# Performance work log

Hardware: AMD Instinct MI355X
Metric: run time of the kernel (lower is better)

The kernel has to match this reference:

```python
import jax, jax.numpy as jnp
import numpy as np

EPS = 1e-5
TAU = 2.0
NUM_HEADS = 8
SCALE = 0.125

# Heaviside spike with sigmoid surrogate gradient (spikingjelly default, alpha=4)
@jax.custom_vjp
def spike_fn(x):
    return (x >= 0).astype(x.dtype)

def _spike_fwd(x):
    return spike_fn(x), x

def _spike_bwd(x, g):
    alpha = 4.0
    s = jax.nn.sigmoid(alpha * x)
    return (g * alpha * s * (1.0 - s),)

spike_fn.defvjp(_spike_fwd, _spike_bwd)

def lif(x, v_th):
    # MultiStepLIFNode: v += (x - v)/tau; spike = H(v - v_th); hard reset v=0 (detach_reset)
    def step(v, xt):
        v = v + (xt - v) / TAU
        s = spike_fn(v - v_th)
        v = v * (1.0 - jax.lax.stop_gradient(s))
        return v, s
    _, s = jax.lax.scan(step, jnp.zeros_like(x[0]), x)
    return s

def bn(y, g, b, m, rv):
    # BatchNorm1d in eval mode over channel dim C (last dim here, since torch code
    # transposes to (TB,C,N) before BN and back after)
    return (y - m) * (g * jax.lax.rsqrt(rv + EPS)) + b

def setup_inputs():
    key = jax.random.key(0)
    T, B, N, C = 4, 8, 512, 512
    ks = jax.random.split(key, 16)
    d = {"x": jax.random.normal(ks[0], (T, B, N, C), jnp.float32)}
    i = 1
    for name in ("q", "k", "v", "p"):
        d[f"w{name}"] = jax.random.normal(ks[i], (C, C), jnp.float32) * 0.02; i += 1
        d[f"b{name}"] = jnp.zeros((C,), jnp.float32)
        d[f"g{name}"] = jnp.ones((C,), jnp.float32)
        d[f"beta{name}"] = jnp.zeros((C,), jnp.float32)
        d[f"m{name}"] = jax.random.normal(ks[i], (C,), jnp.float32) * 0.1; i += 1
        d[f"rv{name}"] = jax.random.uniform(ks[i], (C,), jnp.float32, minval=0.5, maxval=1.5); i += 1
    return d

def reference(x, wq, bq, gq, betaq, mq, rvq,
              wk, bk, gk, betak, mk, rvk,
              wv, bv, gv, betav, mv, rvv,
              wp, bp, gp, betap, mp, rvp):
    T, B, N, C = x.shape
    H = NUM_HEADS
    D = C // H
    xf = x.reshape(T * B, N, C)

    def branch(w, b, g, be, m, rv):
        # Linear -> BN(eval) -> LIF -> split heads
        # (k/v paths in the torch code reshape to (T,B,C,N) between BN and LIF, but
        # since those are pure reshapes of the same flat buffer and LIF is elementwise
        # per timestep, the math is identical to the q path.)
        y = bn(jnp.einsum('bnc,oc->bno', xf, w) + b, g, be, m, rv).reshape(T, B, N, C)
        s = lif(y, 1.0)
        return s.reshape(T, B, N, H, D).transpose(0, 1, 3, 2, 4)  # (T,B,H,N,D)

    q = branch(wq, bq, gq, betaq, mq, rvq)
    k = branch(wk, bk, gk, betak, mk, rvk)
    v = branch(wv, bv, gv, betav, mv, rvv)

    attn = jnp.einsum('tbhnd,tbhmd->tbhnm', q, k) * SCALE  # no softmax
    o = jnp.einsum('tbhnm,tbhmd->tbhnd', attn, v)
    o = o.transpose(0, 1, 3, 2, 4).reshape(T, B, N, C)
    o = lif(o, 0.5)  # attn_lif, v_threshold=0.5

    y = bn(jnp.einsum('bnc,oc->bno', o.reshape(T * B, N, C), wp) + bp,
           gp, betap, mp, rvp).reshape(T, B, N, C)
    return lif(y, 1.0)  # proj_lif
```

## Files before the change

### kernel.cpp

```cpp
#include <hip/hip_runtime.h>
#include <hip/hip_bf16.h>

typedef _Float16 h8 __attribute__((ext_vector_type(8)));
typedef float f4 __attribute__((ext_vector_type(4)));

#define T_ 4
#define B_ 8
#define N_ 512
#define C_ 512
#define H_ 8
#define D_ 64
#define BNR 4096
#define EPSf 1e-5f
#define F16_MIN_NORM 6.1035156e-05f
#define INV4096 0.000244140625f

__global__ __launch_bounds__(256)
void split_pack_x(const float* __restrict__ in, _Float16* __restrict__ h1,
                  _Float16* __restrict__ h2)
{
    const int gid = blockIdx.x * 256 + threadIdx.x;
    const int lane = gid & 63;
    const int ks = (gid >> 6) & 15;
    const int t = (gid >> 10) & 3;
    const int rt = gid >> 12;
    const int row = rt * 16 + (lane & 15);
    const size_t src = ((size_t)t * BNR + row) * C_ + ks * 32 + (lane >> 4) * 8;
    const float4 x0 = *reinterpret_cast<const float4*>(in + src);
    const float4 x1 = *reinterpret_cast<const float4*>(in + src + 4);
    h8 a, b;
    #pragma unroll
    for (int j = 0; j < 8; ++j) {
        const float xv = (j < 4) ? (&x0.x)[j] : (&x1.x)[j - 4];
        const float hi = (fabsf(xv) >= F16_MIN_NORM) ? xv : 0.0f;
        const _Float16 h = (_Float16)hi;
        const float r = (xv - (float)h) * 4096.0f;
        a[j] = h; b[j] = (_Float16)r;
    }
    *reinterpret_cast<h8*>(h1 + (size_t)gid * 8) = a;
    *reinterpret_cast<h8*>(h2 + (size_t)gid * 8) = b;
}

__device__ __forceinline__
void pack_w_one(const float* __restrict__ W, _Float16* __restrict__ Wp1,
                _Float16* __restrict__ Wp2, int gid)
{
    const int lane = gid & 63;
    const int ni = (gid >> 6) & 3;
    const int ks = (gid >> 8) & 15;
    const int ct = gid >> 12;
    const int col = ct * 64 + ni * 16 + (lane & 15);
    const int k = ks * 32 + (lane >> 4) * 8;
    const float* src = W + (size_t)col * C_ + k;
    h8 a, b;
    #pragma unroll
    for (int j = 0; j < 8; ++j) {
        const float xv = src[j];
        const float hi = (fabsf(xv) >= F16_MIN_NORM) ? xv : 0.0f;
        const _Float16 h = (_Float16)hi;
        const float r = (xv - (float)h) * 4096.0f;
        a[j] = h; b[j] = (_Float16)r;
    }
    *reinterpret_cast<h8*>(Wp1 + (size_t)gid * 8) = a;
    *reinterpret_cast<h8*>(Wp2 + (size_t)gid * 8) = b;
}

__global__ __launch_bounds__(256)
void pack_w_all(const float* __restrict__ Wq, const float* __restrict__ Wk,
                const float* __restrict__ Wv, const float* __restrict__ Wp,
                _Float16* q1, _Float16* q2, _Float16* k1, _Float16* k2,
                _Float16* v1, _Float16* v2, _Float16* p1, _Float16* p2)
{
    const int g = blockIdx.x * 256 + threadIdx.x;
    const int br = g >> 15;
    const int gid = g & 32767;
    if (br == 0)      pack_w_one(Wq, q1, q2, gid);
    else if (br == 1) pack_w_one(Wk, k1, k2, gid);
    else if (br == 2) pack_w_one(Wv, v1, v2, gid);
    else              pack_w_one(Wp, p1, p2, gid);
}

__global__ __launch_bounds__(512, 4)
void gemm3_bn_lif(const _Float16* __restrict__ A1p, const _Float16* __restrict__ A2p,
                  const _Float16* __restrict__ Wq1, const _Float16* __restrict__ Wq2,
                  const _Float16* __restrict__ Wk1, const _Float16* __restrict__ Wk2,
                  const _Float16* __restrict__ Wv1, const _Float16* __restrict__ Wv2,
                  const float* __restrict__ biq, const float* __restrict__ gaq,
                  const float* __restrict__ beq, const float* __restrict__ meq,
                  const float* __restrict__ rvq,
                  const float* __restrict__ bik, const float* __restrict__ gak,
                  const float* __restrict__ bek, const float* __restrict__ mek,
                  const float* __restrict__ rvk,
                  const float* __restrict__ biv, const float* __restrict__ gav,
                  const float* __restrict__ bev, const float* __restrict__ mev,
                  const float* __restrict__ rvv,
                  _Float16* __restrict__ oq, _Float16* __restrict__ ok,
                  _Float16* __restrict__ ov)
{
    __shared__ __align__(16) char wsm[16384];
    const int br = blockIdx.y;
    const _Float16* W1 = (br == 0) ? Wq1 : (br == 1) ? Wk1 : Wv1;
    const _Float16* W2 = (br == 0) ? Wq2 : (br == 1) ? Wk2 : Wv2;
    const float* bias = (br == 0) ? biq : (br == 1) ? bik : biv;
    const float* gam  = (br == 0) ? gaq : (br == 1) ? gak : gav;
    const float* bet  = (br == 0) ? beq : (br == 1) ? bek : bev;
    const float* mea  = (br == 0) ? meq : (br == 1) ? mek : mev;
    const float* rva  = (br == 0) ? rvq : (br == 1) ? rvk : rvv;
    _Float16* out = (br == 0) ? oq : (br == 1) ? ok : ov;

    const int id = blockIdx.x;
    const int bt = (id & 7) * 8 + ((id >> 3) & 7);
    const int ct = id >> 6;
    const int tid = threadIdx.x;
    const int wave = tid >> 6, lane = tid & 63;
    const int tp = wave & 1, wr = wave >> 1;
    const int rt = bt * 4 + wr;
    const int row0 = bt * 64, col0 = ct * 64;
    const int lr = lane & 15, lk = lane >> 4;

    f4 accA[2][4], accB[2][4];
    #pragma unroll
    for (int ti = 0; ti < 2; ++ti)
        #pragma unroll
        for (int ni = 0; ni < 4; ++ni) { accA[ti][ni] = (f4)0.0f; accB[ti][ni] = (f4)0.0f; }

    const _Float16* aB1 = A1p + (size_t)rt * 32768 + lane * 8;
    const _Float16* aB2 = A2p + (size_t)rt * 32768 + lane * 8;
    const int s_ = wave >> 2, q_ = wave & 3;
    const _Float16* wsrc = (s_ ? W2 : W1) + (size_t)ct * 32768 + q_ * 512 + lane * 8;
    const int wdoff = s_ * 4096 + q_ * 1024;

    auto stageW = [&](int ks, int b) {
        __builtin_amdgcn_global_load_lds(
            (const __attribute__((address_space(1))) unsigned int*)(wsrc + ks * 2048),
            (__attribute__((address_space(3))) unsigned int*)(wsm + b * 8192 + wdoff),
            16, 0, 0);
    };

    stageW(0, 0);
    h8 a1c[2], a2c[2];
    #pragma unroll
    for (int ti = 0; ti < 2; ++ti) {
        const int t = tp * 2 + ti;
        a1c[ti] = *reinterpret_cast<const h8*>(aB1 + (t * 16 + 0) * 512);
        a2c[ti] = *reinterpret_cast<const h8*>(aB2 + (t * 16 + 0) * 512);
    }
    #pragma unroll
    for (int ks = 0; ks < 16; ++ks) {
        const int buf = ks & 1;
        asm volatile("s_waitcnt vmcnt(4)" ::: "memory");
        __builtin_amdgcn_s_barrier();
        __builtin_amdgcn_sched_barrier(0);
        h8 a1n[2], a2n[2];
        if (ks < 15) {
            stageW(ks + 1, buf ^ 1);
            #pragma unroll
            for (int ti = 0; ti < 2; ++ti) {
                const int t = tp * 2 + ti;
                a1n[ti] = *reinterpret_cast<const h8*>(aB1 + (t * 16 + ks + 1) * 512);
                a2n[ti] = *reinterpret_cast<const h8*>(aB2 + (t * 16 + ks + 1) * 512);
            }
        }
        const char* wb = wsm + buf * 8192;
        #pragma unroll
        for (int ni = 0; ni < 4; ++ni) {
            const h8 wf1 = *reinterpret_cast<const h8*>(wb + ni * 1024 + lane * 16);
            const h8 wf2 = *reinterpret_cast<const h8*>(wb + 4096 + ni * 1024 + lane * 16);
            #pragma unroll
            for (int ti = 0; ti < 2; ++ti) {
                accA[ti][ni] = __builtin_amdgcn_mfma_f32_16x16x32_f16(a1c[ti], wf1, accA[ti][ni], 0, 0, 0);
                accB[ti][ni] = __builtin_amdgcn_mfma_f32_16x16x32_f16(a1c[ti], wf2, accB[ti][ni], 0, 0, 0);
                accB[ti][ni] = __builtin_amdgcn_mfma_f32_16x16x32_f16(a2c[ti], wf1, accB[ti][ni], 0, 0, 0);
            }
        }
        if (ks < 15) {
            #pragma unroll
            for (int ti = 0; ti < 2; ++ti) { a1c[ti] = a1n[ti]; a2c[ti] = a2n[ti]; }
        }
    }

    float* vst = (float*)wsm;
    float sc[4], bi[4], mn[4], be[4];
    #pragma unroll
    for (int ni = 0; ni < 4; ++ni) {
        const int c = col0 + ni * 16 + lr;
        sc[ni] = gam[c] * (1.0f / sqrtf(rva[c] + EPSf));
        bi[ni] = bias[c]; mn[ni] = mea[c]; be[ni] = bet[c];
    }
    __syncthreads();
    if (tp == 0) {
        #pragma unroll
        for (int ni = 0; ni < 4; ++ni)
            #pragma unroll
            for (int r = 0; r < 4; ++r) {
                const int rl = wr * 16 + lk * 4 + r;
                const int bn = row0 + rl;
                float vm = 0.0f;
                #pragma unroll
                for (int ti = 0; ti < 2; ++ti) {
                    const float res = accA[ti][ni][r] + INV4096 * accB[ti][ni][r];
                    const float y = ((res + bi[ni]) - mn[ni]) * sc[ni] + be[ni];
                    vm = vm + (y - vm) * 0.5f;
                    const float s = (vm >= 1.0f) ? 1.0f : 0.0f;
                    vm = (s != 0.0f) ? 0.0f : vm;
                    const int b = bn >> 9, n = bn & 511;
                    out[((((size_t)ti * B_ + b) * H_ + ct) * N_ + n) * D_ + ni * 16 + lr] =
                        (_Float16)s;
                }
                vst[rl * 64 + ni * 16 + lr] = vm;
            }
    }
    __syncthreads();
    if (tp == 1) {
        #pragma unroll
        for (int ni = 0; ni < 4; ++ni)
            #pragma unroll
            for (int r = 0; r < 4; ++r) {
                const int rl = wr * 16 + lk * 4 + r;
                const int bn = row0 + rl;
                float vm = vst[rl * 64 + ni * 16 + lr];
                #pragma unroll
                for (int ti = 0; ti < 2; ++ti) {
                    const float res = accA[ti][ni][r] + INV4096 * accB[ti][ni][r];
                    const float y = ((res + bi[ni]) - mn[ni]) * sc[ni] + be[ni];
                    vm = vm + (y - vm) * 0.5f;
                    const float s = (vm >= 1.0f) ? 1.0f : 0.0f;
                    vm = (s != 0.0f) ? 0.0f : vm;
                    const int b = bn >> 9, n = bn & 511;
                    out[((((size_t)(2 + ti) * B_ + b) * H_ + ct) * N_ + n) * D_ + ni * 16 + lr] =
                        (_Float16)s;
                }
            }
    }
}

__global__ __launch_bounds__(512, 4)
void gemm_p_bn_lif(const _Float16* __restrict__ A1p,
                   const _Float16* __restrict__ Wp1, const _Float16* __restrict__ Wp2,
                   const float* __restrict__ bias, const float* __restrict__ gam,
                   const float* __restrict__ bet, const float* __restrict__ mea,
                   const float* __restrict__ rva, float* __restrict__ out_plain)
{
    __shared__ __align__(16) char wsm[65536];
    const int id = blockIdx.x;
    const int bt = (id & 7) * 8 + ((id >> 3) & 7);
    const int ct = id >> 6;
    const int tid = threadIdx.x;
    const int wave = tid >> 6, lane = tid & 63;
    const int tp = wave & 1, wr = wave >> 1;
    const int rt = bt * 4 + wr;
    const int row0 = bt * 64, col0 = ct * 64;
    const int lr = lane & 15, lk = lane >> 4;

    f4 accA[2][4], accB[2][4];
    #pragma unroll
    for (int ti = 0; ti < 2; ++ti)
        #pragma unroll
        for (int ni = 0; ni < 4; ++ni) { accA[ti][ni] = (f4)0.0f; accB[ti][ni] = (f4)0.0f; }

    const _Float16* aB1 = A1p + (size_t)rt * 32768 + lane * 8;
    const int s_ = wave >> 2, q_ = wave & 3;
    const _Float16* wsrc = (s_ ? Wp2 : Wp1) + (size_t)ct * 32768 + q_ * 512 + lane * 8;
    const int wdoff = s_ * 4096 + q_ * 1024;

    auto stageChunk = [&](int c, int b) {
        #pragma unroll
        for (int ksl = 0; ksl < 4; ++ksl) {
            __builtin_amdgcn_global_load_lds(
                (const __attribute__((address_space(1))) unsigned int*)(wsrc + (c * 4 + ksl) * 2048),
                (__attribute__((address_space(3))) unsigned int*)(wsm + b * 32768 + ksl * 8192 + wdoff),
                16, 0, 0);
        }
    };

    stageChunk(0, 0);
    #pragma unroll
    for (int c = 0; c < 4; ++c) {
        const int buf = c & 1;
        __syncthreads();
        if (c < 3) stageChunk(c + 1, buf ^ 1);
        #pragma unroll
        for (int ksl = 0; ksl < 4; ++ksl) {
            const int ks = c * 4 + ksl;
            h8 a1[2];
            #pragma unroll
            for (int ti = 0; ti < 2; ++ti) {
                const int t = tp * 2 + ti;
                a1[ti] = *reinterpret_cast<const h8*>(aB1 + (t * 16 + ks) * 512);
            }
            const char* wb = wsm + buf * 32768 + ksl * 8192;
            #pragma unroll
            for (int ni = 0; ni < 4; ++ni) {
                const h8 wf1 = *reinterpret_cast<const h8*>(wb + ni * 1024 + lane * 16);
                const h8 wf2 = *reinterpret_cast<const h8*>(wb + 4096 + ni * 1024 + lane * 16);
                #pragma unroll
                for (int ti = 0; ti < 2; ++ti) {
                    accA[ti][ni] = __builtin_amdgcn_mfma_f32_16x16x32_f16(a1[ti], wf1, accA[ti][ni], 0, 0, 0);
                    accB[ti][ni] = __builtin_amdgcn_mfma_f32_16x16x32_f16(a1[ti], wf2, accB[ti][ni], 0, 0, 0);
                }
            }
        }
    }

    float* vst = (float*)wsm;
    float sc[4], bi[4], mn[4], be[4];
    #pragma unroll
    for (int ni = 0; ni < 4; ++ni) {
        const int c = col0 + ni * 16 + lr;
        sc[ni] = gam[c] * (1.0f / sqrtf(rva[c] + EPSf));
        bi[ni] = bias[c]; mn[ni] = mea[c]; be[ni] = bet[c];
    }
    __syncthreads();
    if (tp == 0) {
        #pragma unroll
        for (int ni = 0; ni < 4; ++ni)
            #pragma unroll
            for (int r = 0; r < 4; ++r) {
                const int rl = wr * 16 + lk * 4 + r;
                const int bn = row0 + rl;
                float vm = 0.0f;
                #pragma unroll
                for (int ti = 0; ti < 2; ++ti) {
                    const float res = accA[ti][ni][r] + INV4096 * accB[ti][ni][r];
                    const float y = ((res + bi[ni]) - mn[ni]) * sc[ni] + be[ni];
                    vm = vm + (y - vm) * 0.5f;
                    const float s = (vm >= 1.0f) ? 1.0f : 0.0f;
                    vm = (s != 0.0f) ? 0.0f : vm;
                    out_plain[((size_t)ti * BNR + bn) * C_ + col0 + ni * 16 + lr] = s;
                }
                vst[rl * 64 + ni * 16 + lr] = vm;
            }
    }
    __syncthreads();
    if (tp == 1) {
        #pragma unroll
        for (int ni = 0; ni < 4; ++ni)
            #pragma unroll
            for (int r = 0; r < 4; ++r) {
                const int rl = wr * 16 + lk * 4 + r;
                const int bn = row0 + rl;
                float vm = vst[rl * 64 + ni * 16 + lr];
                #pragma unroll
                for (int ti = 0; ti < 2; ++ti) {
                    const float res = accA[ti][ni][r] + INV4096 * accB[ti][ni][r];
                    const float y = ((res + bi[ni]) - mn[ni]) * sc[ni] + be[ni];
                    vm = vm + (y - vm) * 0.5f;
                    const float s = (vm >= 1.0f) ? 1.0f : 0.0f;
                    vm = (s != 0.0f) ? 0.0f : vm;
                    out_plain[((size_t)(2 + ti) * BNR + bn) * C_ + col0 + ni * 16 + lr] = s;
                }
            }
    }
}

__global__ __launch_bounds__(256)
void ktv_kernel(const _Float16* __restrict__ sk, const _Float16* __restrict__ sv,
                _Float16* __restrict__ kvT)
{
    __shared__ _Float16 kl[64][64];
    __shared__ _Float16 vl[64][64];
    const int tbh = blockIdx.x;
    const int tid = threadIdx.x;
    const int tx = tid & 15, ty = tid >> 4;
    const size_t base = (size_t)tbh * N_ * D_;
    float acc[4][4] = {};
    for (int n0 = 0; n0 < N_; n0 += 64) {
        __syncthreads();
        #pragma unroll
        for (int p = 0; p < 2; ++p) {
            const int idx = tid + p * 256;
            const int r = idx >> 3, c8 = (idx & 7) * 8;
            *reinterpret_cast<float4*>(&kl[r][c8]) =
                *reinterpret_cast<const float4*>(&sk[base + (size_t)(n0 + r) * D_ + c8]);
            *reinterpret_cast<float4*>(&vl[r][c8]) =
                *reinterpret_cast<const float4*>(&sv[base + (size_t)(n0 + r) * D_ + c8]);
        }
        __syncthreads();
        for (int nn = 0; nn < 64; ++nn) {
            float a[4], b[4];
            #pragma unroll
            for (int i = 0; i < 4; ++i) a[i] = (float)kl[nn][ty * 4 + i];
            #pragma unroll
            for (int j = 0; j < 4; ++j) b[j] = (float)vl[nn][tx * 4 + j];
            #pragma unroll
            for (int i = 0; i < 4; ++i)
                #pragma unroll
                for (int j = 0; j < 4; ++j)
                    acc[i][j] = fmaf(a[i], b[j], acc[i][j]);
        }
    }
    _Float16* out = kvT + (size_t)tbh * 4096;
    #pragma unroll
    for (int i = 0; i < 4; ++i)
        #pragma unroll
        for (int j = 0; j < 4; ++j)
            out[(tx * 4 + j) * 64 + ty * 4 + i] = (_Float16)acc[i][j];
}

__global__ __launch_bounds__(256)
void qkv_mfma_lif(const _Float16* __restrict__ sq, const _Float16* __restrict__ kvT,
                  _Float16* __restrict__ osp)
{
    __shared__ __align__(16) char ot[8192];
    const int nt = blockIdx.x, b = blockIdx.y, h = blockIdx.z;
    const int tid = threadIdx.x;
    const int wv = tid >> 6, lane = tid & 63;
    const int lr = lane & 15, lk = lane >> 4;
    const int n0 = nt * 64;

    f4 vst[4];
    #pragma unroll
    for (int ni = 0; ni < 4; ++ni) vst[ni] = (f4)0.0f;

    for (int t = 0; t < T_; ++t) {
        const int tbh = (t * B_ + b) * H_ + h;
        const _Float16* qb = sq + ((size_t)tbh * N_ + n0 + wv * 16 + lr) * D_;
        const h8 a0 = *reinterpret_cast<const h8*>(qb + lk * 8);
        const h8 a1 = *reinterpret_cast<const h8*>(qb + 32 + lk * 8);
        const _Float16* kb = kvT + (size_t)tbh * 4096 + lr * 64 + lk * 8;
        f4 acc[4];
        #pragma unroll
        for (int ni = 0; ni < 4; ++ni) {
            const _Float16* kbn = kb + ni * 1024;
            const h8 b0 = *reinterpret_cast<const h8*>(kbn);
            const h8 b1 = *reinterpret_cast<const h8*>(kbn + 32);
            f4 a = (f4)0.0f;
            a = __builtin_amdgcn_mfma_f32_16x16x32_f16(a0, b0, a, 0, 0, 0);
            a = __builtin_amdgcn_mfma_f32_16x16x32_f16(a1, b1, a, 0, 0, 0);
            acc[ni] = a;
        }
        #pragma unroll
        for (int ni = 0; ni < 4; ++ni)
            #pragma unroll
            for (int r = 0; r < 4; ++r) {
                const float y = 0.125f * acc[ni][r];
                float vv = vst[ni][r];
                vv = vv + (y - vv) * 0.5f;
                const float s = (vv >= 0.5f) ? 1.0f : 0.0f;
                vst[ni][r] = (s != 0.0f) ? 0.0f : vv;
                const int row = wv * 16 + lk * 4 + r;
                const int colb = (ni * 16 + lr) * 2;
                *(_Float16*)(ot + row * 128 + (colb ^ ((row & 7) << 4))) = (_Float16)s;
            }
        const int rt = b * 32 + nt * 4 + wv;
        #pragma unroll
        for (int ks1 = 0; ks1 < 2; ++ks1) {
            const int row = wv * 16 + lr;
            const int colb = ks1 * 64 + lk * 16;
            const h8 vvv = *reinterpret_cast<const h8*>(ot + row * 128 + (colb ^ ((row & 7) << 4)));
            *reinterpret_cast<h8*>(osp +
                ((((size_t)rt * 4 + t) * 16 + h * 2 + ks1) * 64 + lane) * 8) = vvv;
        }
    }
}

extern "C" void kernel_launch(void* const* d_in, const int* in_sizes, int n_in,
                              void* d_out, int out_size, void* d_ws, size_t ws_size,
                              hipStream_t stream)
{
    const float* x = (const float*)d_in[0];
    const float *W[4], *bia[4], *gam[4], *bet[4], *mea[4], *rva[4];
    for (int br = 0; br < 4; ++br) {
        W[br]   = (const float*)d_in[1 + 6 * br + 0];
        bia[br] = (const float*)d_in[1 + 6 * br + 1];
        gam[br] = (const float*)d_in[1 + 6 * br + 2];
        bet[br] = (const float*)d_in[1 + 6 * br + 3];
        mea[br] = (const float*)d_in[1 + 6 * br + 4];
        rva[br] = (const float*)d_in[1 + 6 * br + 5];
    }
    char* ws = (char*)d_ws;
    _Float16* x1 = (_Float16*)(ws + 0);
    _Float16* x2 = (_Float16*)(ws + 16777216);
    _Float16* sq = (_Float16*)(ws + 33554432);
    _Float16* sk = (_Float16*)(ws + 50331648);
    _Float16* sv = (_Float16*)(ws + 67108864);
    _Float16* w1[4], *w2[4];
    for (int br = 0; br < 4; ++br) {
        w1[br] = (_Float16*)(ws + 83886080 + (size_t)br * 1048576);
        w2[br] = (_Float16*)(ws + 83886080 + (size_t)br * 1048576 + 524288);
    }
    _Float16* kvT = (_Float16*)(ws + 16777216);
    _Float16* osp = (_Float16*)(ws + 0);

    dim3 blk(256);
    split_pack_x<<<dim3(4096), blk, 0, stream>>>(x, x1, x2);
    pack_w_all<<<dim3(512), blk, 0, stream>>>(W[0], W[1], W[2], W[3],
        w1[0], w2[0], w1[1], w2[1], w1[2], w2[2], w1[3], w2[3]);

    gemm3_bn_lif<<<dim3(512, 3), dim3(512), 0, stream>>>(x1, x2,
        w1[0], w2[0], w1[1], w2[1], w1[2], w2[2],
        bia[0], gam[0], bet[0], mea[0], rva[0],
        bia[1], gam[1], bet[1], mea[1], rva[1],
        bia[2], gam[2], bet[2], mea[2], rva[2],
        sq, sk, sv);

    ktv_kernel<<<dim3(T_ * B_ * H_), blk, 0, stream>>>(sk, sv, kvT);
    qkv_mfma_lif<<<dim3(N_ / 64, B_, H_), blk, 0, stream>>>(sq, kvT, osp);

    gemm_p_bn_lif<<<dim3(512), dim3(512), 0, stream>>>(osp, w1[3], w2[3],
        bia[3], gam[3], bet[3], mea[3], rva[3], (float*)d_out);
}
```

Measured before the change: 157.9 us.

## Use MFMA for K^T V and finer-grained double-buffered pipeline in projection GEMM

```diff
diff --git a/kernel.cpp b/kernel.cpp
--- a/kernel.cpp
+++ b/kernel.cpp
@@ -241,7 +241,7 @@
                    const float* __restrict__ bet, const float* __restrict__ mea,
                    const float* __restrict__ rva, float* __restrict__ out_plain)
 {
-    __shared__ __align__(16) char wsm[65536];
+    __shared__ __align__(16) char wsm[16384];
     const int id = blockIdx.x;
     const int bt = (id & 7) * 8 + ((id >> 3) & 7);
     const int ct = id >> 6;
@@ -263,42 +263,49 @@
     const _Float16* wsrc = (s_ ? Wp2 : Wp1) + (size_t)ct * 32768 + q_ * 512 + lane * 8;
     const int wdoff = s_ * 4096 + q_ * 1024;
 
-    auto stageChunk = [&](int c, int b) {
-        #pragma unroll
-        for (int ksl = 0; ksl < 4; ++ksl) {
-            __builtin_amdgcn_global_load_lds(
-                (const __attribute__((address_space(1))) unsigned int*)(wsrc + (c * 4 + ksl) * 2048),
-                (__attribute__((address_space(3))) unsigned int*)(wsm + b * 32768 + ksl * 8192 + wdoff),
-                16, 0, 0);
-        }
+    auto stageW = [&](int ks, int b) {
+        __builtin_amdgcn_global_load_lds(
+            (const __attribute__((address_space(1))) unsigned int*)(wsrc + ks * 2048),
+            (__attribute__((address_space(3))) unsigned int*)(wsm + b * 8192 + wdoff),
+            16, 0, 0);
     };
 
-    stageChunk(0, 0);
-    #pragma unroll
-    for (int c = 0; c < 4; ++c) {
-        const int buf = c & 1;
-        __syncthreads();
-        if (c < 3) stageChunk(c + 1, buf ^ 1);
-        #pragma unroll
-        for (int ksl = 0; ksl < 4; ++ksl) {
-            const int ks = c * 4 + ksl;
-            h8 a1[2];
+    stageW(0, 0);
+    h8 a1c[2];
+    #pragma unroll
+    for (int ti = 0; ti < 2; ++ti) {
+        const int t = tp * 2 + ti;
+        a1c[ti] = *reinterpret_cast<const h8*>(aB1 + (t * 16 + 0) * 512);
+    }
+    #pragma unroll
+    for (int ks = 0; ks < 16; ++ks) {
+        const int buf = ks & 1;
+        asm volatile("s_waitcnt vmcnt(2)" ::: "memory");
+        __builtin_amdgcn_s_barrier();
+        __builtin_amdgcn_sched_barrier(0);
+        h8 a1n[2];
+        if (ks < 15) {
+            stageW(ks + 1, buf ^ 1);
             #pragma unroll
             for (int ti = 0; ti < 2; ++ti) {
                 const int t = tp * 2 + ti;
-                a1[ti] = *reinterpret_cast<const h8*>(aB1 + (t * 16 + ks) * 512);
-            }
-            const char* wb = wsm + buf * 32768 + ksl * 8192;
-            #pragma unroll
-            for (int ni = 0; ni < 4; ++ni) {
-                const h8 wf1 = *reinterpret_cast<const h8*>(wb + ni * 1024 + lane * 16);
-                const h8 wf2 = *reinterpret_cast<const h8*>(wb + 4096 + ni * 1024 + lane * 16);
-                #pragma unroll
-                for (int ti = 0; ti < 2; ++ti) {
-                    accA[ti][ni] = __builtin_amdgcn_mfma_f32_16x16x32_f16(a1[ti], wf1, accA[ti][ni], 0, 0, 0);
-                    accB[ti][ni] = __builtin_amdgcn_mfma_f32_16x16x32_f16(a1[ti], wf2, accB[ti][ni], 0, 0, 0);
-                }
-            }
+                a1n[ti] = *reinterpret_cast<const h8*>(aB1 + (t * 16 + ks + 1) * 512);
+            }
+        }
+        const char* wb = wsm + buf * 8192;
+        #pragma unroll
+        for (int ni = 0; ni < 4; ++ni) {
+            const h8 wf1 = *reinterpret_cast<const h8*>(wb + ni * 1024 + lane * 16);
+            const h8 wf2 = *reinterpret_cast<const h8*>(wb + 4096 + ni * 1024 + lane * 16);
+            #pragma unroll
+            for (int ti = 0; ti < 2; ++ti) {
+                accA[ti][ni] = __builtin_amdgcn_mfma_f32_16x16x32_f16(a1c[ti], wf1, accA[ti][ni], 0, 0, 0);
+                accB[ti][ni] = __builtin_amdgcn_mfma_f32_16x16x32_f16(a1c[ti], wf2, accB[ti][ni], 0, 0, 0);
+            }
+        }
+        if (ks < 15) {
+            #pragma unroll
+            for (int ti = 0; ti < 2; ++ti) a1c[ti] = a1n[ti];
         }
     }
 
@@ -354,47 +361,60 @@
 }
 
 __global__ __launch_bounds__(256)
-void ktv_kernel(const _Float16* __restrict__ sk, const _Float16* __restrict__ sv,
-                _Float16* __restrict__ kvT)
-{
-    __shared__ _Float16 kl[64][64];
-    __shared__ _Float16 vl[64][64];
+void ktv_mfma(const _Float16* __restrict__ sk, const _Float16* __restrict__ sv,
+              _Float16* __restrict__ kvT)
+{
+    __shared__ _Float16 kT[64][64];
+    __shared__ _Float16 vT[64][64];
     const int tbh = blockIdx.x;
     const int tid = threadIdx.x;
-    const int tx = tid & 15, ty = tid >> 4;
+    const int wv = tid >> 6, lane = tid & 63;
+    const int lr = lane & 15, lk = lane >> 4;
     const size_t base = (size_t)tbh * N_ * D_;
-    float acc[4][4] = {};
+
+    f4 acc[4];
+    #pragma unroll
+    for (int ni = 0; ni < 4; ++ni) acc[ni] = (f4)0.0f;
+
     for (int n0 = 0; n0 < N_; n0 += 64) {
         __syncthreads();
         #pragma unroll
         for (int p = 0; p < 2; ++p) {
-            const int idx = tid + p * 256;
-            const int r = idx >> 3, c8 = (idx & 7) * 8;
-            *reinterpret_cast<float4*>(&kl[r][c8]) =
-                *reinterpret_cast<const float4*>(&sk[base + (size_t)(n0 + r) * D_ + c8]);
-            *reinterpret_cast<float4*>(&vl[r][c8]) =
-                *reinterpret_cast<const float4*>(&sv[base + (size_t)(n0 + r) * D_ + c8]);
+            const int idx = p * 256 + tid;
+            const int n = idx >> 3, d0 = (idx & 7) * 8;
+            const h8 kv_ = *reinterpret_cast<const h8*>(&sk[base + (size_t)(n0 + n) * D_ + d0]);
+            const h8 vv_ = *reinterpret_cast<const h8*>(&sv[base + (size_t)(n0 + n) * D_ + d0]);
+            #pragma unroll
+            for (int j = 0; j < 8; ++j) {
+                const int d = d0 + j;
+                const int nsw = (((n >> 3) ^ (d & 7)) << 3) | (n & 7);
+                kT[d][nsw] = kv_[j];
+                vT[d][nsw] = vv_[j];
+            }
         }
         __syncthreads();
-        for (int nn = 0; nn < 64; ++nn) {
-            float a[4], b[4];
-            #pragma unroll
-            for (int i = 0; i < 4; ++i) a[i] = (float)kl[nn][ty * 4 + i];
-            #pragma unroll
-            for (int j = 0; j < 4; ++j) b[j] = (float)vl[nn][tx * 4 + j];
-            #pragma unroll
-            for (int i = 0; i < 4; ++i)
-                #pragma unroll
-                for (int j = 0; j < 4; ++j)
-                    acc[i][j] = fmaf(a[i], b[j], acc[i][j]);
+        #pragma unroll
+        for (int ks2 = 0; ks2 < 2; ++ks2) {
+            const int g0 = ks2 * 4 + lk;
+            const int d2 = wv * 16 + lr;
+            const h8 av = *reinterpret_cast<const h8*>(&vT[d2][(g0 ^ (d2 & 7)) << 3]);
+            #pragma unroll
+            for (int ni = 0; ni < 4; ++ni) {
+                const int d1 = ni * 16 + lr;
+                const h8 bk = *reinterpret_cast<const h8*>(&kT[d1][(g0 ^ (d1 & 7)) << 3]);
+                acc[ni] = __builtin_amdgcn_mfma_f32_16x16x32_f16(av, bk, acc[ni], 0, 0, 0);
+            }
         }
     }
     _Float16* out = kvT + (size_t)tbh * 4096;
     #pragma unroll
-    for (int i = 0; i < 4; ++i)
-        #pragma unroll
-        for (int j = 0; j < 4; ++j)
-            out[(tx * 4 + j) * 64 + ty * 4 + i] = (_Float16)acc[i][j];
+    for (int ni = 0; ni < 4; ++ni)
+        #pragma unroll
+        for (int r = 0; r < 4; ++r) {
+            const int d2 = wv * 16 + lk * 4 + r;
+            const int d1 = ni * 16 + lr;
+            out[d2 * 64 + d1] = (_Float16)acc[ni][r];
+        }
 }
 
 __global__ __launch_bounds__(256)
@@ -494,7 +514,7 @@
         bia[2], gam[2], bet[2], mea[2], rva[2],
         sq, sk, sv);
 
-    ktv_kernel<<<dim3(T_ * B_ * H_), blk, 0, stream>>>(sk, sv, kvT);
+    ktv_mfma<<<dim3(T_ * B_ * H_), blk, 0, stream>>>(sk, sv, kvT);
     qkv_mfma_lif<<<dim3(N_ / 64, B_, H_), blk, 0, stream>>>(sq, kvT, osp);
 
     gemm_p_bn_lif<<<dim3(512), dim3(512), 0, stream>>>(osp, w1[3], w2[3],
```

After: 136.8 us. -13.4%, faster.
